# Kernel optimization log

Measured on AMD Instinct MI355X. Metric: run time of the kernel, lower is better.

The kernel has to match this reference:

```python
import jax, jax.numpy as jnp
import numpy as np

N_HEAD = 16
G_HEADS = 2
D_HEAD = 64
D_MODEL = 1024
HEAD_RATIO = N_HEAD // G_HEADS  # 8
QK_DIM = G_HEADS * D_HEAD       # 128
SCALE = 1.0 / D_HEAD ** 0.5
LN_EPS = 1e-5


def _rel_shift(x):
    # x: [qlen, rlen, B, n] -- Transformer-XL relative shift
    q, r = x.shape[0], x.shape[1]
    x_pad = jnp.pad(x, ((0, 0), (1, 0), (0, 0), (0, 0)))      # [q, r+1, B, n]
    x_pad = x_pad.reshape(r + 1, q, *x.shape[2:])[1:]          # drop first row
    return x_pad.reshape(q, r, *x.shape[2:])


def setup_inputs() -> dict:
    key = jax.random.key(0)
    ks = jax.random.split(key, 9)
    qlen, bsz, levels = 1024, 4, 3
    w = jax.random.normal(ks[0], (qlen, bsz, D_MODEL), jnp.float32)
    r = jax.random.normal(ks[1], (qlen, D_MODEL), jnp.float32)
    r_w_bias = jax.random.normal(ks[2], (G_HEADS, D_HEAD), jnp.float32) * 0.02
    r_r_bias = jax.random.normal(ks[3], (G_HEADS, D_HEAD), jnp.float32) * 0.02
    masks = jax.random.uniform(ks[4], (qlen, qlen, levels), jnp.float32)
    W_qkv = jax.random.normal(ks[5], (2 * QK_DIM + N_HEAD * D_HEAD, D_MODEL), jnp.float32) * 0.02
    W_r = jax.random.normal(ks[6], (QK_DIM, D_MODEL), jnp.float32) * 0.02
    mask_proj = jnp.ones((levels, N_HEAD), jnp.float32)
    W_o = jax.random.normal(ks[7], (D_MODEL, N_HEAD * D_HEAD), jnp.float32) * 0.02
    ln_gamma = jnp.ones((D_MODEL,), jnp.float32)
    ln_beta = jnp.zeros((D_MODEL,), jnp.float32)
    return dict(w=w, r=r, r_w_bias=r_w_bias, r_r_bias=r_r_bias, masks=masks,
                W_qkv=W_qkv, W_r=W_r, mask_proj=mask_proj, W_o=W_o,
                ln_gamma=ln_gamma, ln_beta=ln_beta)


def reference(w, r, r_w_bias, r_r_bias, masks, W_qkv, W_r, mask_proj, W_o, ln_gamma, ln_beta):
    qlen, bsz, _ = w.shape
    rlen = r.shape[0]
    N = qlen  # no mems: klen == qlen == rlen

    w_heads = w @ W_qkv.T                                   # [q, B, 1280]
    r_head_k = (r @ W_r.T).reshape(rlen, G_HEADS, D_HEAD)   # [r, gH, d]
    w_head_q = w_heads[..., :QK_DIM].reshape(qlen, bsz, G_HEADS, D_HEAD)
    w_head_k = w_heads[..., QK_DIM:2 * QK_DIM].reshape(qlen, bsz, G_HEADS, D_HEAD)
    w_head_v = w_heads[..., 2 * QK_DIM:].reshape(qlen, bsz, N_HEAD, D_HEAD)

    AC = jnp.einsum('ibnd,jbnd->ijbn', w_head_q + r_w_bias, w_head_k)
    BD = jnp.einsum('ibnd,jnd->ijbn', w_head_q + r_r_bias, r_head_k)
    BD = _rel_shift(BD)
    attn_score = (AC + BD) * SCALE                           # [N, N, B, gH]

    # per-head mask mixing ('full' projection)
    attn = jnp.transpose(attn_score, (2, 3, 0, 1))           # [B, gH, N, N]
    mw = (masks @ mask_proj).reshape(N, N, G_HEADS, HEAD_RATIO)
    mw = jnp.transpose(mw, (2, 0, 1, 3))                     # [gH, N, N, hr]
    attn = attn[..., None] * mw[None]                        # [B, gH, N, N, hr]
    attn = jnp.transpose(attn, (0, 1, 4, 2, 3)).reshape(bsz, N_HEAD, N, N)
    attn_score = jnp.transpose(attn, (2, 3, 0, 1))           # [N, N, B, H]

    attn_prob = jax.nn.softmax(attn_score, axis=1)
    attn_vec = jnp.einsum('ijbn,jbnd->ibnd', attn_prob, w_head_v)
    attn_vec = attn_vec.reshape(qlen, bsz, N_HEAD * D_HEAD)
    attn_out = attn_vec @ W_o.T                              # [q, B, d_model]

    # post-LN residual
    x = w + attn_out
    mu = jnp.mean(x, axis=-1, keepdims=True)
    var = jnp.mean((x - mu) ** 2, axis=-1, keepdims=True)
    return (x - mu) * jax.lax.rsqrt(var + LN_EPS) * ln_gamma + ln_beta
```

## Files before the change

kernel.cpp:

```cpp
#include <hip/hip_runtime.h>
#include <cstddef>
#include <cstdint>

#define QLEN   1024
#define SCALE  0.125f
#define LN_EPS 1e-5f
#define DMODEL 1024

typedef __bf16 bf16x8 __attribute__((ext_vector_type(8)));
typedef __bf16 bf16x4 __attribute__((ext_vector_type(4)));
typedef float  f32x4  __attribute__((ext_vector_type(4)));

__device__ __forceinline__ void load16_lds(const void* g, void* l) {
  __builtin_amdgcn_global_load_lds(
      (const __attribute__((address_space(1))) unsigned int*)g,
      (__attribute__((address_space(3))) unsigned int*)l, 16, 0, 0);
}

__global__ __launch_bounds__(256) void cast_all(
    const float* __restrict__ w, __bf16* __restrict__ w_bf,
    const float* __restrict__ Wqkv, __bf16* __restrict__ Wqkv_bf,
    const float* __restrict__ r, __bf16* __restrict__ r_bf,
    const float* __restrict__ Wr, __bf16* __restrict__ Wr_bf,
    const float* __restrict__ Wo, __bf16* __restrict__ Wo_bf)
{
  int blk = blockIdx.x;
  const float* in; __bf16* out;
  if (blk < 2048)      { in = w;    out = w_bf;    }
  else if (blk < 2688) { blk -= 2048; in = Wqkv; out = Wqkv_bf; }
  else if (blk < 3200) { blk -= 2688; in = r;    out = r_bf;    }
  else if (blk < 3264) { blk -= 3200; in = Wr;   out = Wr_bf;   }
  else                 { blk -= 3264; in = Wo;   out = Wo_bf;   }
  const size_t i = ((size_t)blk * 256 + threadIdx.x) * 8;
  const float4 a = *(const float4*)&in[i];
  const float4 b = *(const float4*)&in[i + 4];
  bf16x8 o;
  o[0] = (__bf16)a.x; o[1] = (__bf16)a.y; o[2] = (__bf16)a.z; o[3] = (__bf16)a.w;
  o[4] = (__bf16)b.x; o[5] = (__bf16)b.y; o[6] = (__bf16)b.z; o[7] = (__bf16)b.w;
  *(bf16x8*)&out[i] = o;
}

__global__ __launch_bounds__(256) void gemm_proj(
    const __bf16* __restrict__ w_bf, const __bf16* __restrict__ Wqkv_bf,
    const __bf16* __restrict__ r_bf, const __bf16* __restrict__ Wr_bf,
    const float* __restrict__ rwb, const float* __restrict__ rrb,
    __bf16* __restrict__ Qw, __bf16* __restrict__ Qr,
    __bf16* __restrict__ Kb, __bf16* __restrict__ Vt,
    __bf16* __restrict__ Rb)
{
  __shared__ __bf16 Asl[128 * 32];
  __shared__ __bf16 Bsl[64 * 32];
  const int blk = blockIdx.x;
  const bool isR = blk >= 640;
  const __bf16 *A, *B;
  int m0, n0;
  if (!isR) { A = w_bf; B = Wqkv_bf; n0 = (blk % 20) * 64; m0 = (blk / 20) * 128; }
  else      { const int k = blk - 640; A = r_bf; B = Wr_bf;
              n0 = (k % 2) * 64; m0 = (k / 2) * 128; }

  const int tid = threadIdx.x, lane = tid & 63, wv = tid >> 6;
  const int lr = lane & 15, kq = lane >> 4;
  const int srow  = wv * 16 + (lane >> 2);
  const int sslot = lane & 3;
  const int sg0 = (sslot - ((srow >> 1) & 3)) & 3;
  const int sg1 = (sslot - (((srow + 64) >> 1) & 3)) & 3;
  const __bf16* Ag = A + (size_t)(m0 + srow) * 1024;
  const __bf16* Bg = B + (size_t)(n0 + srow) * 1024;
  __bf16* Al = &Asl[srow * 32 + sslot * 8];
  __bf16* Bl = &Bsl[srow * 32 + sslot * 8];

  f32x4 acc[2][4];
#pragma unroll
  for (int mt = 0; mt < 2; ++mt)
#pragma unroll
    for (int nt = 0; nt < 4; ++nt)
      acc[mt][nt] = (f32x4){0.f, 0.f, 0.f, 0.f};

  for (int k0 = 0; k0 < 1024; k0 += 32) {
    load16_lds(Ag + k0 + sg0 * 8, Al);
    load16_lds(Ag + (size_t)64 * 1024 + k0 + sg1 * 8, Al + 64 * 32);
    load16_lds(Bg + k0 + sg0 * 8, Bl);
    __syncthreads();
    bf16x8 af[2], bfr[4];
#pragma unroll
    for (int mt = 0; mt < 2; ++mt) {
      const int row = wv * 32 + mt * 16 + lr;
      af[mt] = *(const bf16x8*)&Asl[row * 32 + ((kq + (row >> 1)) & 3) * 8];
    }
#pragma unroll
    for (int nt = 0; nt < 4; ++nt) {
      const int row = nt * 16 + lr;
      bfr[nt] = *(const bf16x8*)&Bsl[row * 32 + ((kq + (row >> 1)) & 3) * 8];
    }
#pragma unroll
    for (int mt = 0; mt < 2; ++mt)
#pragma unroll
      for (int nt = 0; nt < 4; ++nt)
        acc[mt][nt] = __builtin_amdgcn_mfma_f32_16x16x32_bf16(
            af[mt], bfr[nt], acc[mt][nt], 0, 0, 0);
    __syncthreads();
  }

#pragma unroll
  for (int mt = 0; mt < 2; ++mt) {
    const int row0 = m0 + wv * 32 + mt * 16 + kq * 4;
#pragma unroll
    for (int nt = 0; nt < 4; ++nt) {
      const int gcol = n0 + nt * 16 + lr;
      const f32x4 c = acc[mt][nt];
      if (isR) {
        const int g = gcol >> 6, d = gcol & 63;
#pragma unroll
        for (int reg = 0; reg < 4; ++reg)
          Rb[(size_t)g * 65536 + (size_t)(row0 + reg) * 64 + d] = (__bf16)c[reg];
      } else if (gcol < 128) {
        const int g = gcol >> 6, d = gcol & 63;
        const float bw = rwb[gcol], br = rrb[gcol];
#pragma unroll
        for (int reg = 0; reg < 4; ++reg) {
          const int row = row0 + reg, i = row >> 2, b = row & 3;
          const size_t o = (size_t)(b * 2 + g) * 65536 + (size_t)i * 64 + d;
          Qw[o] = (__bf16)(c[reg] + bw);
          Qr[o] = (__bf16)(c[reg] + br);
        }
      } else if (gcol < 256) {
        const int lc = gcol - 128, g = lc >> 6, d = lc & 63;
#pragma unroll
        for (int reg = 0; reg < 4; ++reg) {
          const int row = row0 + reg, i = row >> 2, b = row & 3;
          Kb[(size_t)(b * 2 + g) * 65536 + (size_t)i * 64 + d] = (__bf16)c[reg];
        }
      } else {
        const int lc = gcol - 256, h = lc >> 6, d = lc & 63;
#pragma unroll
        for (int reg = 0; reg < 4; ++reg) {
          const int row = row0 + reg, i = row >> 2, b = row & 3;
          Vt[((size_t)((b * 16 + h) * 64 + d)) * 1024 + i] = (__bf16)c[reg];
        }
      }
    }
  }
}

__global__ __launch_bounds__(256) void gemm_wo(
    const __bf16* __restrict__ A, const __bf16* __restrict__ B,
    float* __restrict__ C)
{
  __shared__ __bf16 Asl[128 * 32];
  __shared__ __bf16 Bsl[64 * 32];
  const int m0 = blockIdx.y * 128, n0 = blockIdx.x * 64;
  const int tid = threadIdx.x, lane = tid & 63, wv = tid >> 6;
  const int lr = lane & 15, kq = lane >> 4;
  const int srow  = wv * 16 + (lane >> 2);
  const int sslot = lane & 3;
  const int sg0 = (sslot - ((srow >> 1) & 3)) & 3;
  const int sg1 = (sslot - (((srow + 64) >> 1) & 3)) & 3;
  const __bf16* Ag = A + (size_t)(m0 + srow) * 1024;
  const __bf16* Bg = B + (size_t)(n0 + srow) * 1024;
  __bf16* Al = &Asl[srow * 32 + sslot * 8];
  __bf16* Bl = &Bsl[srow * 32 + sslot * 8];

  f32x4 acc[2][4];
#pragma unroll
  for (int mt = 0; mt < 2; ++mt)
#pragma unroll
    for (int nt = 0; nt < 4; ++nt)
      acc[mt][nt] = (f32x4){0.f, 0.f, 0.f, 0.f};

  for (int k0 = 0; k0 < 1024; k0 += 32) {
    load16_lds(Ag + k0 + sg0 * 8, Al);
    load16_lds(Ag + (size_t)64 * 1024 + k0 + sg1 * 8, Al + 64 * 32);
    load16_lds(Bg + k0 + sg0 * 8, Bl);
    __syncthreads();
    bf16x8 af[2], bfr[4];
#pragma unroll
    for (int mt = 0; mt < 2; ++mt) {
      const int row = wv * 32 + mt * 16 + lr;
      af[mt] = *(const bf16x8*)&Asl[row * 32 + ((kq + (row >> 1)) & 3) * 8];
    }
#pragma unroll
    for (int nt = 0; nt < 4; ++nt) {
      const int row = nt * 16 + lr;
      bfr[nt] = *(const bf16x8*)&Bsl[row * 32 + ((kq + (row >> 1)) & 3) * 8];
    }
#pragma unroll
    for (int mt = 0; mt < 2; ++mt)
#pragma unroll
      for (int nt = 0; nt < 4; ++nt)
        acc[mt][nt] = __builtin_amdgcn_mfma_f32_16x16x32_bf16(
            af[mt], bfr[nt], acc[mt][nt], 0, 0, 0);
    __syncthreads();
  }

#pragma unroll
  for (int mt = 0; mt < 2; ++mt) {
    const int row0 = m0 + wv * 32 + mt * 16 + kq * 4;
#pragma unroll
    for (int nt = 0; nt < 4; ++nt) {
      const int col = n0 + nt * 16 + lr;
      const f32x4 c = acc[mt][nt];
#pragma unroll
      for (int reg = 0; reg < 4; ++reg)
        C[(size_t)(row0 + reg) * 1024 + col] = c[reg];
    }
  }
}

__global__ __launch_bounds__(256) void gemm64_bf16(
    const __bf16* __restrict__ Qw, const __bf16* __restrict__ Qr,
    const __bf16* __restrict__ Kb, const __bf16* __restrict__ Rb,
    __bf16* __restrict__ AC, __bf16* __restrict__ BDo)
{
  __shared__ __bf16 Asl[128 * 64];
  __shared__ __bf16 Bsl[128 * 64];
  const int tid = threadIdx.x, lane = tid & 63, wv = tid >> 6;
  const int which = blockIdx.z & 1, bat = blockIdx.z >> 1;
  const int m0 = blockIdx.y * 128, n0 = blockIdx.x * 128;
  const __bf16* Ap = (which ? Qr : Qw) + (size_t)bat * 65536;
  const __bf16* Bp = which ? (Rb + (size_t)(bat & 1) * 65536)
                           : (Kb + (size_t)bat * 65536);
  __bf16* Cp = (which ? BDo : AC) + (size_t)bat * 1048576;

#pragma unroll
  for (int p = 0; p < 4; ++p) {
    const int row = wv * 32 + p * 8 + (lane >> 3);
    const int s = lane & 7;
    const int gc = (s - (row & 7)) & 7;
    load16_lds(Ap + (size_t)(m0 + row) * 64 + gc * 8, &Asl[row * 64 + s * 8]);
    load16_lds(Bp + (size_t)(n0 + row) * 64 + gc * 8, &Bsl[row * 64 + s * 8]);
  }
  __syncthreads();

  const int lr = lane & 15, kq = lane >> 4;
  const int wm = (wv >> 1) * 64, wn = (wv & 1) * 64;
  f32x4 acc[4][4];
#pragma unroll
  for (int mt = 0; mt < 4; ++mt)
#pragma unroll
    for (int nt = 0; nt < 4; ++nt)
      acc[mt][nt] = (f32x4){0.f, 0.f, 0.f, 0.f};

#pragma unroll
  for (int ks = 0; ks < 2; ++ks) {
    const int c = ks * 4 + kq;
    bf16x8 af[4], bfr[4];
#pragma unroll
    for (int mt = 0; mt < 4; ++mt) {
      const int row = wm + mt * 16 + lr;
      af[mt] = *(const bf16x8*)&Asl[row * 64 + ((c + (row & 7)) & 7) * 8];
    }
#pragma unroll
    for (int nt = 0; nt < 4; ++nt) {
      const int row = wn + nt * 16 + lr;
      bfr[nt] = *(const bf16x8*)&Bsl[row * 64 + ((c + (row & 7)) & 7) * 8];
    }
#pragma unroll
    for (int mt = 0; mt < 4; ++mt)
#pragma unroll
      for (int nt = 0; nt < 4; ++nt)
        acc[mt][nt] = __builtin_amdgcn_mfma_f32_16x16x32_bf16(
            af[mt], bfr[nt], acc[mt][nt], 0, 0, 0);
  }

#pragma unroll
  for (int mt = 0; mt < 4; ++mt) {
    const int row0 = m0 + wm + mt * 16 + kq * 4;
#pragma unroll
    for (int nt = 0; nt < 4; ++nt) {
      const int col = n0 + wn + nt * 16 + lr;
      const f32x4 cc = acc[mt][nt];
#pragma unroll
      for (int reg = 0; reg < 4; ++reg)
        Cp[(size_t)(row0 + reg) * 1024 + col] = (__bf16)cc[reg];
    }
  }
}

__global__ __launch_bounds__(256) void prep2(
    const __bf16* __restrict__ AC, const __bf16* __restrict__ BDm,
    __bf16* __restrict__ Tg,
    const float* __restrict__ masks, const float* __restrict__ mproj,
    __bf16* __restrict__ Mh)
{
  const int tid = threadIdx.x;
  if (blockIdx.x < 2048) {
    const int blk = blockIdx.x;
    const size_t bg = blk >> 8;
    const int i = (blk & 255) * 4 + (tid >> 6);
    const int lane = tid & 63;
    const __bf16* ACr = AC + bg * 1048576 + (size_t)i * 1024;
    const __bf16* BDb = BDm + bg * 1048576;
    __bf16* Tr = Tg + bg * 1048576 + (size_t)i * 1024;
#pragma unroll
    for (int c2 = 0; c2 < 4; ++c2) {
      const int j0 = c2 * 256 + lane * 4;
      const bf16x4 ac4 = *(const bf16x4*)&ACr[j0];
      bf16x4 o;
#pragma unroll
      for (int k = 0; k < 4; ++k) {
        const int j = j0 + k;
        float bd;
        if (j <= i)          bd = (float)BDb[(size_t)i * 1024 + (j + QLEN - 1 - i)];
        else if (j == i + 1) bd = 0.f;
        else                 bd = (float)BDb[(size_t)(i + 1) * 1024 + (j - i - 2)];
        o[k] = (__bf16)(((float)ac4[k] + bd) * SCALE);
      }
      *(bf16x4*)&Tr[j0] = o;
    }
  } else {
    const int blk = blockIdx.x - 2048;
    const size_t ij0 = ((size_t)blk * 256 + tid) * 4;
    const float4 a = *(const float4*)&masks[ij0 * 3];
    const float4 b = *(const float4*)&masks[ij0 * 3 + 4];
    const float4 c = *(const float4*)&masks[ij0 * 3 + 8];
    const float m0[4] = {a.x, a.w, b.z, c.y};
    const float m1[4] = {a.y, b.x, b.w, c.z};
    const float m2[4] = {a.z, b.y, c.x, c.w};
#pragma unroll
    for (int h = 0; h < 16; ++h) {
      const float p0 = mproj[h], p1 = mproj[16 + h], p2 = mproj[32 + h];
      bf16x4 o;
#pragma unroll
      for (int k = 0; k < 4; ++k)
        o[k] = (__bf16)(m0[k] * p0 + m1[k] * p1 + m2[k] * p2);
      *(bf16x4*)&Mh[(size_t)h * 1048576 + ij0] = o;
    }
  }
}

__global__ __launch_bounds__(256) void attn6(
    const __bf16* __restrict__ Tg, const __bf16* __restrict__ Mh,
    const __bf16* __restrict__ Vt, __bf16* __restrict__ av)
{
  __shared__ __bf16 P[16 * 1024];
  __shared__ float rinvS[16];
  const int tid = threadIdx.x;
  const int i0 = blockIdx.x * 16;
  const int h = blockIdx.y, b = blockIdx.z;
  const int g = h >> 3;
  const size_t bg = (size_t)(b * 2 + g);
  const int r = tid >> 4, li = tid & 15;
  const __bf16* Trow = Tg + bg * 1048576 + (size_t)(i0 + r) * 1024;
  const __bf16* Mrow = Mh + (size_t)h * 1048576 + (size_t)(i0 + r) * 1024;

  float sum = 0.f;
#pragma unroll
  for (int q = 0; q < 8; ++q) {
    const int jb = q * 128 + li * 8;
    const bf16x8 t8 = *(const bf16x8*)&Trow[jb];
    const bf16x8 m8 = *(const bf16x8*)&Mrow[jb];
    const int csw = (jb >> 3) ^ (r & 7);
    bf16x8 p8;
#pragma unroll
    for (int k = 0; k < 8; ++k) {
      const float e = __expf((float)t8[k] * (float)m8[k]);
      sum += e;
      p8[k] = (__bf16)e;
    }
    *(bf16x8*)&P[r * 1024 + csw * 8] = p8;
  }
  sum += __shfl_xor(sum, 1);
  sum += __shfl_xor(sum, 2);
  sum += __shfl_xor(sum, 4);
  sum += __shfl_xor(sum, 8);
  if (li == 0) rinvS[r] = 1.f / sum;
  __syncthreads();

  const int lane = tid & 63, wv = tid >> 6;
  const int m = lane & 15, kq = lane >> 4;
  const __bf16* vbase = Vt + ((size_t)((b * 16 + h) * 64 + wv * 16 + m)) * 1024 + kq * 8;
  f32x4 acc[4];
#pragma unroll
  for (int u = 0; u < 4; ++u) acc[u] = (f32x4){0.f, 0.f, 0.f, 0.f};
#pragma unroll 2
  for (int ks = 0; ks < 32; ks += 4) {
#pragma unroll
    for (int u = 0; u < 4; ++u) {
      const int c = (ks + u) * 4 + kq;
      const bf16x8 a = *(const bf16x8*)&P[m * 1024 + ((c ^ (m & 7)) << 3)];
      const bf16x8 vv = *(const bf16x8*)&vbase[(ks + u) * 32];
      acc[u] = __builtin_amdgcn_mfma_f32_16x16x32_bf16(a, vv, acc[u], 0, 0, 0);
    }
  }
  const f32x4 accf = (acc[0] + acc[1]) + (acc[2] + acc[3]);
#pragma unroll
  for (int reg = 0; reg < 4; ++reg) {
    const int row = kq * 4 + reg;
    av[((size_t)(i0 + row) * 4 + b) * 1024 + h * 64 + wv * 16 + m] =
        (__bf16)(accf[reg] * rinvS[row]);
  }
}

__global__ __launch_bounds__(256) void ln_kernel(
    const float* __restrict__ w, const float* __restrict__ ao,
    const float* __restrict__ gamma, const float* __restrict__ beta,
    float* __restrict__ out)
{
  const int tid = threadIdx.x;
  const size_t base = (size_t)blockIdx.x * DMODEL;
  __shared__ float red[256];
  float x[4];
  float s = 0.f;
#pragma unroll
  for (int p = 0; p < 4; ++p) {
    const int c = tid + p * 256;
    x[p] = w[base + c] + ao[base + c];
    s += x[p];
  }
  red[tid] = s; __syncthreads();
  for (int off = 128; off > 0; off >>= 1) {
    if (tid < off) red[tid] += red[tid + off];
    __syncthreads();
  }
  const float mu = red[0] * (1.f / DMODEL);
  __syncthreads();
  float s2 = 0.f;
#pragma unroll
  for (int p = 0; p < 4; ++p) { const float t = x[p] - mu; s2 += t * t; }
  red[tid] = s2; __syncthreads();
  for (int off = 128; off > 0; off >>= 1) {
    if (tid < off) red[tid] += red[tid + off];
    __syncthreads();
  }
  const float rs = rsqrtf(red[0] * (1.f / DMODEL) + LN_EPS);
#pragma unroll
  for (int p = 0; p < 4; ++p) {
    const int c = tid + p * 256;
    out[base + c] = (x[p] - mu) * rs * gamma[c] + beta[c];
  }
}

extern "C" void kernel_launch(void* const* d_in, const int* in_sizes, int n_in,
                              void* d_out, int out_size, void* d_ws, size_t ws_size,
                              hipStream_t stream)
{
  const float* w     = (const float*)d_in[0];
  const float* r     = (const float*)d_in[1];
  const float* rwb   = (const float*)d_in[2];
  const float* rrb   = (const float*)d_in[3];
  const float* masks = (const float*)d_in[4];
  const float* Wqkv  = (const float*)d_in[5];
  const float* Wr    = (const float*)d_in[6];
  const float* mproj = (const float*)d_in[7];
  const float* Wo    = (const float*)d_in[8];
  const float* gam   = (const float*)d_in[9];
  const float* bet   = (const float*)d_in[10];
  float* out = (float*)d_out;

  float* ws = (float*)d_ws;
  __bf16* w_bf    = (__bf16*)(ws);
  __bf16* Wqkv_bf = (__bf16*)(ws + 2097152);
  __bf16* r_bf    = (__bf16*)(ws + 2752512);
  __bf16* Wr_bf   = (__bf16*)(ws + 3276800);
  __bf16* Qw      = (__bf16*)(ws + 3342336);
  __bf16* Qr      = (__bf16*)(ws + 3604480);
  __bf16* Kb      = (__bf16*)(ws + 3866624);
  __bf16* Rb      = (__bf16*)(ws + 4128768);
  __bf16* Mh      = (__bf16*)(ws);
  __bf16* AC_bf   = (__bf16*)(ws + 8388608);
  float*  ao      = ws + 8388608;
  __bf16* BD_bf   = (__bf16*)(ws + 12582912);
  __bf16* Tg      = (__bf16*)(ws + 16777216);
  __bf16* Vt      = (__bf16*)(ws + 20971520);
  __bf16* av_bf   = (__bf16*)(ws + 23068672);
  __bf16* Wo_bf   = (__bf16*)(ws + 25165824);

  cast_all<<<3776, 256, 0, stream>>>(w, w_bf, Wqkv, Wqkv_bf, r, r_bf,
                                     Wr, Wr_bf, Wo, Wo_bf);
  gemm_proj<<<656, 256, 0, stream>>>(
      w_bf, Wqkv_bf, r_bf, Wr_bf, rwb, rrb, Qw, Qr, Kb, Vt, Rb);
  gemm64_bf16<<<dim3(8, 8, 16), 256, 0, stream>>>(Qw, Qr, Kb, Rb, AC_bf, BD_bf);
  prep2<<<3072, 256, 0, stream>>>(AC_bf, BD_bf, Tg, masks, mproj, Mh);
  attn6<<<dim3(64, 16, 4), 256, 0, stream>>>(Tg, Mh, Vt, av_bf);
  gemm_wo<<<dim3(16, 32), 256, 0, stream>>>(av_bf, Wo_bf, ao);
  ln_kernel<<<4096, 256, 0, stream>>>(w, ao, gam, bet, out);
}
```

Measured before the change: 266.3 us.

## Chunk attention softmax-PV over keys with double-buffered LDS probabilities

The attention kernel now processes the 1024 keys in four 256-wide chunks. Each chunk's exponentials are written into one of two LDS buffers, and the PV MFMAs for that chunk run before the next chunk is computed, with one lightweight barrier per chunk. This interleaves the memory-bound exp stage with matrix work instead of running them as two separate phases. It also halves LDS use and adds a launch-bounds occupancy hint so more blocks can be resident. The cost is extra barriers and shorter MFMA bursts per chunk.

Measured after the change: 260.8 us. -2.0%, faster.

```diff
diff --git a/kernel.cpp b/kernel.cpp
--- a/kernel.cpp
+++ b/kernel.cpp
@@ -15,6 +15,12 @@
   __builtin_amdgcn_global_load_lds(
       (const __attribute__((address_space(1))) unsigned int*)g,
       (__attribute__((address_space(3))) unsigned int*)l, 16, 0, 0);
+}
+
+__device__ __forceinline__ void bar_lds() {
+  asm volatile("s_waitcnt lgkmcnt(0)" ::: "memory");
+  __builtin_amdgcn_s_barrier();
+  asm volatile("" ::: "memory");
 }
 
 __global__ __launch_bounds__(256) void cast_all(
@@ -328,11 +334,11 @@
   }
 }
 
-__global__ __launch_bounds__(256) void attn6(
+__global__ __launch_bounds__(256, 8) void attn7(
     const __bf16* __restrict__ Tg, const __bf16* __restrict__ Mh,
     const __bf16* __restrict__ Vt, __bf16* __restrict__ av)
 {
-  __shared__ __bf16 P[16 * 1024];
+  __shared__ __bf16 P[2][16 * 256];
   __shared__ float rinvS[16];
   const int tid = threadIdx.x;
   const int i0 = blockIdx.x * 16;
@@ -343,22 +349,42 @@
   const __bf16* Trow = Tg + bg * 1048576 + (size_t)(i0 + r) * 1024;
   const __bf16* Mrow = Mh + (size_t)h * 1048576 + (size_t)(i0 + r) * 1024;
 
+  const int lane = tid & 63, wv = tid >> 6;
+  const int m = lane & 15, kq = lane >> 4;
+  const __bf16* vbase = Vt + ((size_t)((b * 16 + h) * 64 + wv * 16 + m)) * 1024 + kq * 8;
+
   float sum = 0.f;
-#pragma unroll
-  for (int q = 0; q < 8; ++q) {
-    const int jb = q * 128 + li * 8;
-    const bf16x8 t8 = *(const bf16x8*)&Trow[jb];
-    const bf16x8 m8 = *(const bf16x8*)&Mrow[jb];
-    const int csw = (jb >> 3) ^ (r & 7);
-    bf16x8 p8;
-#pragma unroll
-    for (int k = 0; k < 8; ++k) {
-      const float e = __expf((float)t8[k] * (float)m8[k]);
-      sum += e;
-      p8[k] = (__bf16)e;
-    }
-    *(bf16x8*)&P[r * 1024 + csw * 8] = p8;
-  }
+  f32x4 acc[4];
+#pragma unroll
+  for (int u = 0; u < 4; ++u) acc[u] = (f32x4){0.f, 0.f, 0.f, 0.f};
+
+  for (int ch = 0; ch < 4; ++ch) {
+    const int cb = ch & 1;
+#pragma unroll
+    for (int q = 0; q < 2; ++q) {
+      const int jc = q * 128 + li * 8;
+      const bf16x8 t8 = *(const bf16x8*)&Trow[ch * 256 + jc];
+      const bf16x8 m8 = *(const bf16x8*)&Mrow[ch * 256 + jc];
+      const int slot = (jc >> 3) ^ (r & 7);
+      bf16x8 p8;
+#pragma unroll
+      for (int k = 0; k < 8; ++k) {
+        const float e = __expf((float)t8[k] * (float)m8[k]);
+        sum += e;
+        p8[k] = (__bf16)e;
+      }
+      *(bf16x8*)&P[cb][r * 256 + slot * 8] = p8;
+    }
+    bar_lds();
+#pragma unroll
+    for (int ks = 0; ks < 8; ++ks) {
+      const int c = ks * 4 + kq;
+      const bf16x8 a = *(const bf16x8*)&P[cb][m * 256 + ((c ^ (m & 7)) << 3)];
+      const bf16x8 vv = *(const bf16x8*)&vbase[(ch * 8 + ks) * 32];
+      acc[ks & 3] = __builtin_amdgcn_mfma_f32_16x16x32_bf16(a, vv, acc[ks & 3], 0, 0, 0);
+    }
+  }
+
   sum += __shfl_xor(sum, 1);
   sum += __shfl_xor(sum, 2);
   sum += __shfl_xor(sum, 4);
@@ -366,22 +392,6 @@
   if (li == 0) rinvS[r] = 1.f / sum;
   __syncthreads();
 
-  const int lane = tid & 63, wv = tid >> 6;
-  const int m = lane & 15, kq = lane >> 4;
-  const __bf16* vbase = Vt + ((size_t)((b * 16 + h) * 64 + wv * 16 + m)) * 1024 + kq * 8;
-  f32x4 acc[4];
-#pragma unroll
-  for (int u = 0; u < 4; ++u) acc[u] = (f32x4){0.f, 0.f, 0.f, 0.f};
-#pragma unroll 2
-  for (int ks = 0; ks < 32; ks += 4) {
-#pragma unroll
-    for (int u = 0; u < 4; ++u) {
-      const int c = (ks + u) * 4 + kq;
-      const bf16x8 a = *(const bf16x8*)&P[m * 1024 + ((c ^ (m & 7)) << 3)];
-      const bf16x8 vv = *(const bf16x8*)&vbase[(ks + u) * 32];
-      acc[u] = __builtin_amdgcn_mfma_f32_16x16x32_bf16(a, vv, acc[u], 0, 0, 0);
-    }
-  }
   const f32x4 accf = (acc[0] + acc[1]) + (acc[2] + acc[3]);
 #pragma unroll
   for (int reg = 0; reg < 4; ++reg) {
@@ -471,7 +481,7 @@
       w_bf, Wqkv_bf, r_bf, Wr_bf, rwb, rrb, Qw, Qr, Kb, Vt, Rb);
   gemm64_bf16<<<dim3(8, 8, 16), 256, 0, stream>>>(Qw, Qr, Kb, Rb, AC_bf, BD_bf);
   prep2<<<3072, 256, 0, stream>>>(AC_bf, BD_bf, Tg, masks, mproj, Mh);
-  attn6<<<dim3(64, 16, 4), 256, 0, stream>>>(Tg, Mh, Vt, av_bf);
+  attn7<<<dim3(64, 16, 4), 256, 0, stream>>>(Tg, Mh, Vt, av_bf);
   gemm_wo<<<dim3(16, 32), 256, 0, stream>>>(av_bf, Wo_bf, ao);
   ln_kernel<<<4096, 256, 0, stream>>>(w, ao, gam, bet, out);
 }
```
